# Performance work log

Measured on AMD Instinct MI355X. Metric: run time of the kernel, lower is better.

## Reference

```python
import jax, jax.numpy as jnp
import numpy as np

B, T, E = 2, 2048, 768
H = 12
HD = E // H          # 64
ROT = 32             # rotary dim (= head_dim // 2 in CLVP)
SCALE = HD ** -0.5


def rotate_half(x):
    # split last dim into (2, d/2), rotate second half by 90 deg
    x = x.reshape(*x.shape[:-1], 2, x.shape[-1] // 2)
    x1, x2 = x[..., 0, :], x[..., 1, :]
    return jnp.concatenate([-x2, x1], axis=-1)


def apply_rotary_pos_emb(state, freqs):
    # state: (B*H, T, HD); freqs: (1, T, ROT)
    pos_emb_len = freqs.shape[-1]
    s_l, s_r = state[..., :pos_emb_len], state[..., pos_emb_len:]
    f = freqs[:, :, -s_l.shape[-1]:]
    s_l = s_l * jnp.cos(f) + rotate_half(s_l) * jnp.sin(f)
    return jnp.concatenate([s_l, s_r], axis=-1)


def setup_inputs() -> dict:
    key = jax.random.key(0)
    ks = jax.random.split(key, 6)
    hidden_states = jax.random.normal(ks[0], (B, T, E), dtype=jnp.float32)
    rotary_pos_emb = jax.random.uniform(ks[1], (1, T, ROT), dtype=jnp.float32)
    Wq = jax.random.normal(ks[2], (E, E), dtype=jnp.float32) * 0.02
    Wk = jax.random.normal(ks[3], (E, E), dtype=jnp.float32) * 0.02
    Wv = jax.random.normal(ks[4], (E, E), dtype=jnp.float32) * 0.02
    Wo = jax.random.normal(ks[5], (E, E), dtype=jnp.float32) * 0.02
    bo = jnp.zeros((E,), dtype=jnp.float32)
    return {"hidden_states": hidden_states, "rotary_pos_emb": rotary_pos_emb,
            "Wq": Wq, "Wk": Wk, "Wv": Wv, "Wo": Wo, "bo": bo}


def _shape(x):
    # (B, T, E) -> (B*H, T, HD)
    return x.reshape(B, T, H, HD).transpose(0, 2, 1, 3).reshape(B * H, T, HD)


def reference(hidden_states, rotary_pos_emb, Wq, Wk, Wv, Wo, bo):
    # nn.Linear: x @ W.T
    q = _shape(hidden_states @ Wq.T * SCALE)
    k = _shape(hidden_states @ Wk.T)
    v = _shape(hidden_states @ Wv.T)

    q = apply_rotary_pos_emb(q, rotary_pos_emb)
    k = apply_rotary_pos_emb(k, rotary_pos_emb)
    v = apply_rotary_pos_emb(v, rotary_pos_emb)  # CLVP applies RoPE to V too

    attn = jax.nn.softmax(jnp.einsum('bqd,bkd->bqk', q, k), axis=-1)  # (B*H, T, T)
    out = jnp.einsum('bqk,bkd->bqd', attn, v)                          # (B*H, T, HD)
    out = out.reshape(B, H, T, HD).transpose(0, 2, 1, 3).reshape(B, T, E)
    return out @ Wo.T + bo
```

## Files before the change

kernel.cpp:

```cpp
#include <hip/hip_runtime.h>
#include <hip/hip_bf16.h>

typedef unsigned short ushort_t;
typedef __attribute__((ext_vector_type(8))) short short8;
typedef __attribute__((ext_vector_type(4))) float f32x4;

constexpr int B  = 2;
constexpr int T  = 2048;
constexpr int E  = 768;
constexpr int H  = 12;
constexpr int HD = 64;

__device__ __forceinline__ ushort_t f2bf(float x) {
  unsigned int u = __float_as_uint(x);
  u += 0x7fffu + ((u >> 16) & 1u);
  return (ushort_t)(u >> 16);
}

__device__ __forceinline__ unsigned int pack_bf2(float a, float b) {
  __hip_bfloat162 h = __float22bfloat162_rn(float2{a, b});
  return *(unsigned int*)&h;
}

__device__ __forceinline__ int swz(int row, int col) {
  return row * 64 + ((((col >> 3) ^ (row & 7)) << 3) | (col & 7));
}
__device__ __forceinline__ int swz32(int row, int col) {
  return row * 32 + ((((col >> 3) ^ (row & 3)) << 3) | (col & 7));
}

__global__ __launch_bounds__(256) void cvt_all(
    const float* __restrict__ X,  const float* __restrict__ Wq,
    const float* __restrict__ Wk, const float* __restrict__ Wv,
    const float* __restrict__ Wo, const float* __restrict__ rope,
    ushort_t* __restrict__ Xb,  ushort_t* __restrict__ Wqb,
    ushort_t* __restrict__ Wkb, ushort_t* __restrict__ Wvb,
    ushort_t* __restrict__ Wob, float* __restrict__ ct, float* __restrict__ st)
{
  constexpr int NX4 = (B * T * E) / 4;
  constexpr int NW4 = (E * E) / 4;
  constexpr int NC4 = NX4 + 4 * NW4;
  int i = blockIdx.x * 256 + threadIdx.x;
  if (i < NC4) {
    const float* s; ushort_t* d; int j;
    if (i < NX4) { s = X; d = Xb; j = i; }
    else {
      int t = i - NX4;
      int w = t / NW4; j = t - w * NW4;
      s = (w == 0) ? Wq : (w == 1) ? Wk : (w == 2) ? Wv : Wo;
      d = (w == 0) ? Wqb : (w == 1) ? Wkb : (w == 2) ? Wvb : Wob;
    }
    float4 v = ((const float4*)s)[j];
    ushort4 o;
    o.x = f2bf(v.x); o.y = f2bf(v.y); o.z = f2bf(v.z); o.w = f2bf(v.w);
    ((ushort4*)d)[j] = o;
  } else {
    int j = (i - NC4) * 4;
    float4 f = *(const float4*)(rope + j);
    float c, s;
    sincosf(f.x, &s, &c); ct[j+0] = c; st[j+0] = s;
    sincosf(f.y, &s, &c); ct[j+1] = c; st[j+1] = s;
    sincosf(f.z, &s, &c); ct[j+2] = c; st[j+2] = s;
    sincosf(f.w, &s, &c); ct[j+3] = c; st[j+3] = s;
  }
}

__global__ __launch_bounds__(256) void qkv_gemm(
    const ushort_t* __restrict__ Xb,
    const ushort_t* __restrict__ Wqb, const ushort_t* __restrict__ Wkb,
    const ushort_t* __restrict__ Wvb,
    const float* __restrict__ ct, const float* __restrict__ st,
    ushort_t* __restrict__ qb, ushort_t* __restrict__ kb, ushort_t* __restrict__ vtb)
{
  __shared__ __align__(16) ushort_t smem[64 * 132];
  ushort_t* Xs = smem;
  ushort_t* Ws = smem + 128 * 32;
  const int tid  = threadIdx.x;
  const int wave = tid >> 6;
  const int lane = tid & 63;
  const int l15  = lane & 15, quad = lane >> 4;
  const int n0 = blockIdx.x * 64;
  const int m0 = blockIdx.y * 128;
  const int z  = blockIdx.z;
  const ushort_t* Wt = (z == 0) ? Wqb : (z == 1) ? Wkb : Wvb;
  const int h = n0 >> 6;

  f32x4 acc[2][4];
  #pragma unroll
  for (int i = 0; i < 2; ++i)
    #pragma unroll
    for (int j = 0; j < 4; ++j) acc[i][j] = (f32x4){0.f, 0.f, 0.f, 0.f};

  const int srX = tid >> 1, scX = (tid & 1) * 16;
  const int srW = tid >> 2, scW = (tid & 3) * 8;

  for (int k0 = 0; k0 < E; k0 += 32) {
    uint4 xa = *(const uint4*)(Xb + (size_t)(m0 + srX) * E + k0 + scX);
    uint4 xc = *(const uint4*)(Xb + (size_t)(m0 + srX) * E + k0 + scX + 8);
    uint4 wa = *(const uint4*)(Wt + (size_t)(n0 + srW) * E + k0 + scW);
    *(uint4*)&Xs[swz32(srX, scX)]     = xa;
    *(uint4*)&Xs[swz32(srX, scX + 8)] = xc;
    *(uint4*)&Ws[swz32(srW, scW)]     = wa;
    __syncthreads();
    short8 a[2];
    #pragma unroll
    for (int mt = 0; mt < 2; ++mt)
      a[mt] = *(const short8*)&Xs[swz32(wave * 32 + mt * 16 + l15, quad * 8)];
    #pragma unroll
    for (int nt = 0; nt < 4; ++nt) {
      short8 bb = *(const short8*)&Ws[swz32(nt * 16 + l15, quad * 8)];
      #pragma unroll
      for (int mt = 0; mt < 2; ++mt)
        acc[mt][nt] = __builtin_amdgcn_mfma_f32_16x16x32_bf16(a[mt], bb, acc[mt][nt], 0, 0, 0);
    }
    __syncthreads();
  }

  const float qscale = (z == 0) ? 0.125f : 1.0f;
  if (z < 2) {
    #pragma unroll
    for (int mt = 0; mt < 2; ++mt) {
      #pragma unroll
      for (int r = 0; r < 4; ++r) {
        int mloc = wave * 32 + mt * 16 + quad * 4 + r;
        int t = (m0 + mloc) & (T - 1);
        float s0 = acc[mt][0][r] * qscale;
        float s1 = acc[mt][1][r] * qscale;
        float c0v = ct[t * 32 + l15],      sn0 = st[t * 32 + l15];
        float c1v = ct[t * 32 + 16 + l15], sn1 = st[t * 32 + 16 + l15];
        smem[mloc * 64 + l15]      = f2bf(s0 * c0v - s1 * sn0);
        smem[mloc * 64 + 16 + l15] = f2bf(s1 * c1v + s0 * sn1);
        smem[mloc * 64 + 32 + l15] = f2bf(acc[mt][2][r] * qscale);
        smem[mloc * 64 + 48 + l15] = f2bf(acc[mt][3][r] * qscale);
      }
    }
    __syncthreads();
    ushort_t* dst = (z == 0) ? qb : kb;
    int row = tid >> 1, half = (tid & 1) * 32;
    int m = m0 + row, b = m >> 11, t = m & (T - 1);
    size_t base = ((size_t)(b * H + h) * T + t) * HD + half;
    #pragma unroll
    for (int c = 0; c < 32; c += 8)
      *(uint4*)(dst + base + c) = *(const uint4*)&smem[row * 64 + half + c];
  } else {
    #pragma unroll
    for (int mt = 0; mt < 2; ++mt) {
      #pragma unroll
      for (int r = 0; r < 4; ++r) {
        int mloc = wave * 32 + mt * 16 + quad * 4 + r;
        int t = (m0 + mloc) & (T - 1);
        float s0 = acc[mt][0][r], s1 = acc[mt][1][r];
        float c0v = ct[t * 32 + l15],      sn0 = st[t * 32 + l15];
        float c1v = ct[t * 32 + 16 + l15], sn1 = st[t * 32 + 16 + l15];
        smem[(l15)      * 132 + mloc] = f2bf(s0 * c0v - s1 * sn0);
        smem[(16 + l15) * 132 + mloc] = f2bf(s1 * c1v + s0 * sn1);
        smem[(32 + l15) * 132 + mloc] = f2bf(acc[mt][2][r]);
        smem[(48 + l15) * 132 + mloc] = f2bf(acc[mt][3][r]);
      }
    }
    __syncthreads();
    int b = m0 >> 11, t0 = m0 & (T - 1);
    int d = tid >> 2, c0 = (tid & 3) * 32;
    size_t obase = ((size_t)(b * H + h) * HD + d) * (size_t)T + t0 + c0;
    #pragma unroll
    for (int c = 0; c < 32; c += 8)
      *(uint4*)(vtb + obase + c) = *(const uint4*)&smem[d * 132 + c0 + c];
  }
}

__global__ __launch_bounds__(256, 4) void attn_kernel(
    const ushort_t* __restrict__ qbuf, const ushort_t* __restrict__ kbuf,
    const ushort_t* __restrict__ vtbuf, ushort_t* __restrict__ cbuf)
{
  __shared__ __align__(16) ushort_t Ks[2][64 * 64];
  __shared__ __align__(16) ushort_t Vt[2][64 * 64];
  __shared__ __align__(16) ushort_t Ps[64 * 64];
  const int tid  = threadIdx.x;
  const int wave = tid >> 6;
  const int lane = tid & 63;
  const int l15  = lane & 15, quad = lane >> 4;
  const int q0 = blockIdx.x * 64;
  const int bh = blockIdx.y;
  const ushort_t* Qg = qbuf  + (size_t)bh * T * HD;
  const ushort_t* Kg = kbuf  + (size_t)bh * T * HD;
  const ushort_t* Vg = vtbuf + (size_t)bh * HD * T;

  short8 qa[2];
  #pragma unroll
  for (int hf = 0; hf < 2; ++hf)
    qa[hf] = *(const short8*)(Qg + (size_t)(q0 + wave * 16 + l15) * HD + hf * 32 + quad * 8);

  const int srow = tid >> 2, cb0 = (tid & 3) * 16;
  {
    uint4 ka = *(const uint4*)(Kg + (size_t)srow * HD + cb0);
    uint4 kc = *(const uint4*)(Kg + (size_t)srow * HD + cb0 + 8);
    uint4 va = *(const uint4*)(Vg + (size_t)srow * T + cb0);
    uint4 vc = *(const uint4*)(Vg + (size_t)srow * T + cb0 + 8);
    *(uint4*)&Ks[0][swz(srow, cb0)]     = ka;
    *(uint4*)&Ks[0][swz(srow, cb0 + 8)] = kc;
    *(uint4*)&Vt[0][swz(srow, cb0)]     = va;
    *(uint4*)&Vt[0][swz(srow, cb0 + 8)] = vc;
  }
  __syncthreads();

  f32x4 o[4];
  #pragma unroll
  for (int nt = 0; nt < 4; ++nt) o[nt] = (f32x4){0.f, 0.f, 0.f, 0.f};
  float lsum = 0.f;

  for (int kt = 0; kt < T; kt += 64) {
    const int cur = (kt >> 6) & 1;
    const bool more = (kt + 64) < T;
    uint4 nk0, nk1, nv0, nv1;
    if (more) {
      nk0 = *(const uint4*)(Kg + (size_t)(kt + 64 + srow) * HD + cb0);
      nk1 = *(const uint4*)(Kg + (size_t)(kt + 64 + srow) * HD + cb0 + 8);
      nv0 = *(const uint4*)(Vg + (size_t)srow * T + kt + 64 + cb0);
      nv1 = *(const uint4*)(Vg + (size_t)srow * T + kt + 64 + cb0 + 8);
    }

    f32x4 ss[4];
    #pragma unroll
    for (int mt = 0; mt < 4; ++mt) ss[mt] = (f32x4){0.f, 0.f, 0.f, 0.f};
    #pragma unroll
    for (int mt = 0; mt < 4; ++mt) {
      int row = mt * 16 + l15;
      short8 ka0 = *(const short8*)&Ks[cur][swz(row, quad * 8)];
      short8 ka1 = *(const short8*)&Ks[cur][swz(row, 32 + quad * 8)];
      ss[mt] = __builtin_amdgcn_mfma_f32_16x16x32_bf16(ka0, qa[0], ss[mt], 0, 0, 0);
      ss[mt] = __builtin_amdgcn_mfma_f32_16x16x32_bf16(ka1, qa[1], ss[mt], 0, 0, 0);
    }

    const int rp = wave * 16 + l15;
    #pragma unroll
    for (int mt = 0; mt < 4; ++mt) {
      float p0 = __expf(ss[mt][0]);
      float p1 = __expf(ss[mt][1]);
      float p2 = __expf(ss[mt][2]);
      float p3 = __expf(ss[mt][3]);
      lsum += (p0 + p1) + (p2 + p3);
      uint2 w2;
      w2.x = pack_bf2(p0, p1);
      w2.y = pack_bf2(p2, p3);
      *(uint2*)&Ps[swz(rp, mt * 16 + quad * 4)] = w2;
    }

    short8 pa0 = *(const short8*)&Ps[swz(rp, quad * 8)];
    short8 pa1 = *(const short8*)&Ps[swz(rp, 32 + quad * 8)];
    #pragma unroll
    for (int nt = 0; nt < 4; ++nt) {
      int vr = nt * 16 + l15;
      short8 vb0 = *(const short8*)&Vt[cur][swz(vr, quad * 8)];
      short8 vb1 = *(const short8*)&Vt[cur][swz(vr, 32 + quad * 8)];
      o[nt] = __builtin_amdgcn_mfma_f32_16x16x32_bf16(pa0, vb0, o[nt], 0, 0, 0);
      o[nt] = __builtin_amdgcn_mfma_f32_16x16x32_bf16(pa1, vb1, o[nt], 0, 0, 0);
    }

    if (more) {
      const int nxt = cur ^ 1;
      *(uint4*)&Ks[nxt][swz(srow, cb0)]     = nk0;
      *(uint4*)&Ks[nxt][swz(srow, cb0 + 8)] = nk1;
      *(uint4*)&Vt[nxt][swz(srow, cb0)]     = nv0;
      *(uint4*)&Vt[nxt][swz(srow, cb0 + 8)] = nv1;
    }
    __syncthreads();
  }

  lsum += __shfl_xor(lsum, 16);
  lsum += __shfl_xor(lsum, 32);

  const int b = bh / H, h = bh % H;
  #pragma unroll
  for (int r = 0; r < 4; ++r) {
    float lr = __shfl(lsum, quad * 4 + r);
    float inv = 1.0f / lr;
    int t = q0 + wave * 16 + quad * 4 + r;
    size_t base = ((size_t)b * T + t) * E + h * HD;
    cbuf[base + l15]      = f2bf(o[0][r] * inv);
    cbuf[base + 16 + l15] = f2bf(o[1][r] * inv);
    cbuf[base + 32 + l15] = f2bf(o[2][r] * inv);
    cbuf[base + 48 + l15] = f2bf(o[3][r] * inv);
  }
}

__global__ __launch_bounds__(256) void out_gemm(
    const ushort_t* __restrict__ Xc, const ushort_t* __restrict__ Wob,
    const float* __restrict__ bo, float* __restrict__ out)
{
  __shared__ __align__(16) ushort_t Xs[128][40];
  __shared__ __align__(16) ushort_t Ws[64][40];
  const int tid  = threadIdx.x;
  const int wave = tid >> 6;
  const int lane = tid & 63;
  const int l15  = lane & 15, quad = lane >> 4;
  const int n0 = blockIdx.x * 64;
  const int m0 = blockIdx.y * 128;

  f32x4 acc[2][4];
  #pragma unroll
  for (int i = 0; i < 2; ++i)
    #pragma unroll
    for (int j = 0; j < 4; ++j) acc[i][j] = (f32x4){0.f, 0.f, 0.f, 0.f};

  const int srX = tid >> 1, scX = (tid & 1) * 16;
  const int srW = tid >> 2, scW = (tid & 3) * 8;

  for (int k0 = 0; k0 < E; k0 += 32) {
    *(uint4*)&Xs[srX][scX]     = *(const uint4*)(Xc + (size_t)(m0 + srX) * E + k0 + scX);
    *(uint4*)&Xs[srX][scX + 8] = *(const uint4*)(Xc + (size_t)(m0 + srX) * E + k0 + scX + 8);
    *(uint4*)&Ws[srW][scW]     = *(const uint4*)(Wob + (size_t)(n0 + srW) * E + k0 + scW);
    __syncthreads();
    #pragma unroll
    for (int mt = 0; mt < 2; ++mt) {
      short8 a = *(const short8*)&Xs[wave * 32 + mt * 16 + l15][quad * 8];
      #pragma unroll
      for (int nt = 0; nt < 4; ++nt) {
        short8 bb = *(const short8*)&Ws[nt * 16 + l15][quad * 8];
        acc[mt][nt] = __builtin_amdgcn_mfma_f32_16x16x32_bf16(a, bb, acc[mt][nt], 0, 0, 0);
      }
    }
    __syncthreads();
  }

  float bias[4];
  #pragma unroll
  for (int nt = 0; nt < 4; ++nt) bias[nt] = bo[n0 + nt * 16 + l15];
  #pragma unroll
  for (int mt = 0; mt < 2; ++mt) {
    #pragma unroll
    for (int r = 0; r < 4; ++r) {
      int m = m0 + wave * 32 + mt * 16 + quad * 4 + r;
      float* op = out + (size_t)m * E + n0;
      op[l15]      = acc[mt][0][r] + bias[0];
      op[16 + l15] = acc[mt][1][r] + bias[1];
      op[32 + l15] = acc[mt][2][r] + bias[2];
      op[48 + l15] = acc[mt][3][r] + bias[3];
    }
  }
}

extern "C" void kernel_launch(void* const* d_in, const int* in_sizes, int n_in,
                              void* d_out, int out_size, void* d_ws, size_t ws_size,
                              hipStream_t stream) {
  (void)in_sizes; (void)n_in; (void)out_size; (void)ws_size;
  const float* X    = (const float*)d_in[0];
  const float* rope = (const float*)d_in[1];
  const float* Wq   = (const float*)d_in[2];
  const float* Wk   = (const float*)d_in[3];
  const float* Wv   = (const float*)d_in[4];
  const float* Wo   = (const float*)d_in[5];
  const float* bo   = (const float*)d_in[6];
  float* out = (float*)d_out;

  const size_t NX = (size_t)B * T * E;
  const size_t NW = (size_t)E * E;
  const size_t NR = (size_t)T * 32;
  ushort_t* Xb  = (ushort_t*)d_ws;
  ushort_t* Wqb = Xb  + NX;
  ushort_t* Wkb = Wqb + NW;
  ushort_t* Wvb = Wkb + NW;
  ushort_t* Wob = Wvb + NW;
  ushort_t* qb  = Wob + NW;
  ushort_t* kb  = qb  + NX;
  ushort_t* vtb = kb  + NX;
  ushort_t* cb  = vtb + NX;
  float* ct = (float*)(cb + NX);
  float* st = ct + NR;

  const int total4 = (int)((NX + 4 * NW + NR) / 4);
  cvt_all<<<total4 / 256, 256, 0, stream>>>(X, Wq, Wk, Wv, Wo, rope,
                                            Xb, Wqb, Wkb, Wvb, Wob, ct, st);

  qkv_gemm<<<dim3(E / 64, (B * T) / 128, 3), 256, 0, stream>>>(
      Xb, Wqb, Wkb, Wvb, ct, st, qb, kb, vtb);
  attn_kernel<<<dim3(T / 64, B * H), 256, 0, stream>>>(qb, kb, vtb, cb);
  out_gemm<<<dim3(E / 64, (B * T) / 128), 256, 0, stream>>>(cb, Wob, bo, out);
}
```

Baseline: 183.2 us.

## Store Q/K/V in MFMA fragment order and load attention operands directly to registers

The QKV GEMM epilogue now writes Q, K and V in a pre-swizzled per-lane MFMA fragment layout. This lets the attention kernel load its operands with coalesced 16-byte global loads straight into registers, instead of staging K and V through double-buffered shared memory. Block-wide barriers and most LDS traffic in the attention loop go away, leaving only a per-wave P buffer. In exchange, each wave re-reads K/V from global memory or L2 on its own, with no sharing within the block, and register pressure goes up from prefetching the next K tile.

```diff
diff --git a/kernel.cpp b/kernel.cpp
--- a/kernel.cpp
+++ b/kernel.cpp
@@ -70,7 +70,7 @@
     const ushort_t* __restrict__ Wqb, const ushort_t* __restrict__ Wkb,
     const ushort_t* __restrict__ Wvb,
     const float* __restrict__ ct, const float* __restrict__ st,
-    ushort_t* __restrict__ qb, ushort_t* __restrict__ kb, ushort_t* __restrict__ vtb)
+    ushort_t* __restrict__ qfb, ushort_t* __restrict__ kfb, ushort_t* __restrict__ vfb)
 {
   __shared__ __align__(16) ushort_t smem[64 * 132];
   ushort_t* Xs = smem;
@@ -116,7 +116,11 @@
     __syncthreads();
   }
 
+  const int b  = m0 >> 11;
+  const int t0 = m0 & (T - 1);
+  const int bh = b * H + h;
   const float qscale = (z == 0) ? 0.125f : 1.0f;
+
   if (z < 2) {
     #pragma unroll
     for (int mt = 0; mt < 2; ++mt) {
@@ -128,20 +132,36 @@
         float s1 = acc[mt][1][r] * qscale;
         float c0v = ct[t * 32 + l15],      sn0 = st[t * 32 + l15];
         float c1v = ct[t * 32 + 16 + l15], sn1 = st[t * 32 + 16 + l15];
-        smem[mloc * 64 + l15]      = f2bf(s0 * c0v - s1 * sn0);
-        smem[mloc * 64 + 16 + l15] = f2bf(s1 * c1v + s0 * sn1);
-        smem[mloc * 64 + 32 + l15] = f2bf(acc[mt][2][r] * qscale);
-        smem[mloc * 64 + 48 + l15] = f2bf(acc[mt][3][r] * qscale);
-      }
-    }
-    __syncthreads();
-    ushort_t* dst = (z == 0) ? qb : kb;
-    int row = tid >> 1, half = (tid & 1) * 32;
-    int m = m0 + row, b = m >> 11, t = m & (T - 1);
-    size_t base = ((size_t)(b * H + h) * T + t) * HD + half;
-    #pragma unroll
-    for (int c = 0; c < 32; c += 8)
-      *(uint4*)(dst + base + c) = *(const uint4*)&smem[row * 64 + half + c];
+        smem[swz(mloc, l15)]      = f2bf(s0 * c0v - s1 * sn0);
+        smem[swz(mloc, 16 + l15)] = f2bf(s1 * c1v + s0 * sn1);
+        smem[swz(mloc, 32 + l15)] = f2bf(acc[mt][2][r] * qscale);
+        smem[swz(mloc, 48 + l15)] = f2bf(acc[mt][3][r] * qscale);
+      }
+    }
+    __syncthreads();
+    if (z == 0) {
+      #pragma unroll
+      for (int i = 0; i < 4; ++i) {
+        int p = tid + 256 * i;
+        int qtl = p >> 7, kh = (p >> 6) & 1, ln = p & 63;
+        int tl = qtl * 16 + (ln & 15);
+        int d  = kh * 32 + (ln >> 4) * 8;
+        uint4 v = *(const uint4*)&smem[swz(tl, d)];
+        size_t off = ((size_t)((bh * 128 + (t0 >> 4) + qtl) * 2 + kh)) * 512 + ln * 8;
+        *(uint4*)(qfb + off) = v;
+      }
+    } else {
+      #pragma unroll
+      for (int i = 0; i < 4; ++i) {
+        int p = tid + 256 * i;
+        int ktl = p >> 9, mt = (p >> 7) & 3, kh = (p >> 6) & 1, ln = p & 63;
+        int tl = ktl * 64 + mt * 16 + (ln & 15);
+        int d  = kh * 32 + (ln >> 4) * 8;
+        uint4 v = *(const uint4*)&smem[swz(tl, d)];
+        size_t off = ((size_t)(((bh * 32 + (t0 >> 6) + ktl) * 4 + mt) * 2 + kh)) * 512 + ln * 8;
+        *(uint4*)(kfb + off) = v;
+      }
+    }
   } else {
     #pragma unroll
     for (int mt = 0; mt < 2; ++mt) {
@@ -159,79 +179,75 @@
       }
     }
     __syncthreads();
-    int b = m0 >> 11, t0 = m0 & (T - 1);
-    int d = tid >> 2, c0 = (tid & 3) * 32;
-    size_t obase = ((size_t)(b * H + h) * HD + d) * (size_t)T + t0 + c0;
-    #pragma unroll
-    for (int c = 0; c < 32; c += 8)
-      *(uint4*)(vtb + obase + c) = *(const uint4*)&smem[d * 132 + c0 + c];
-  }
-}
-
-__global__ __launch_bounds__(256, 4) void attn_kernel(
-    const ushort_t* __restrict__ qbuf, const ushort_t* __restrict__ kbuf,
-    const ushort_t* __restrict__ vtbuf, ushort_t* __restrict__ cbuf)
+    #pragma unroll
+    for (int i = 0; i < 4; ++i) {
+      int p = tid + 256 * i;
+      int ktl = p >> 9, nt = (p >> 7) & 3, kh = (p >> 6) & 1, ln = p & 63;
+      int d  = nt * 16 + (ln & 15);
+      int tl = ktl * 64 + kh * 32 + (ln >> 4) * 8;
+      uint4 v = *(const uint4*)&smem[d * 132 + tl];
+      size_t off = ((size_t)(((bh * 32 + (t0 >> 6) + ktl) * 4 + nt) * 2 + kh)) * 512 + ln * 8;
+      *(uint4*)(vfb + off) = v;
+    }
+  }
+}
+
+__global__ __launch_bounds__(256) void attn_kernel(
+    const ushort_t* __restrict__ qfb, const ushort_t* __restrict__ kfb,
+    const ushort_t* __restrict__ vfb, ushort_t* __restrict__ cbuf)
 {
-  __shared__ __align__(16) ushort_t Ks[2][64 * 64];
-  __shared__ __align__(16) ushort_t Vt[2][64 * 64];
-  __shared__ __align__(16) ushort_t Ps[64 * 64];
+  __shared__ __align__(16) ushort_t Ps[4][16 * 64];
   const int tid  = threadIdx.x;
   const int wave = tid >> 6;
   const int lane = tid & 63;
   const int l15  = lane & 15, quad = lane >> 4;
   const int q0 = blockIdx.x * 64;
   const int bh = blockIdx.y;
-  const ushort_t* Qg = qbuf  + (size_t)bh * T * HD;
-  const ushort_t* Kg = kbuf  + (size_t)bh * T * HD;
-  const ushort_t* Vg = vtbuf + (size_t)bh * HD * T;
+  const ushort_t* Qf = qfb + (size_t)bh * (T * HD);
+  const ushort_t* Kf = kfb + (size_t)bh * (T * HD);
+  const ushort_t* Vf = vfb + (size_t)bh * (T * HD);
+  ushort_t* Pw = &Ps[wave][0];
 
   short8 qa[2];
   #pragma unroll
-  for (int hf = 0; hf < 2; ++hf)
-    qa[hf] = *(const short8*)(Qg + (size_t)(q0 + wave * 16 + l15) * HD + hf * 32 + quad * 8);
-
-  const int srow = tid >> 2, cb0 = (tid & 3) * 16;
-  {
-    uint4 ka = *(const uint4*)(Kg + (size_t)srow * HD + cb0);
-    uint4 kc = *(const uint4*)(Kg + (size_t)srow * HD + cb0 + 8);
-    uint4 va = *(const uint4*)(Vg + (size_t)srow * T + cb0);
-    uint4 vc = *(const uint4*)(Vg + (size_t)srow * T + cb0 + 8);
-    *(uint4*)&Ks[0][swz(srow, cb0)]     = ka;
-    *(uint4*)&Ks[0][swz(srow, cb0 + 8)] = kc;
-    *(uint4*)&Vt[0][swz(srow, cb0)]     = va;
-    *(uint4*)&Vt[0][swz(srow, cb0 + 8)] = vc;
-  }
-  __syncthreads();
+  for (int kh = 0; kh < 2; ++kh)
+    qa[kh] = *(const short8*)(Qf + ((size_t)(((q0 >> 4) + wave) * 2 + kh)) * 512 + lane * 8);
+
+  short8 ka[4][2];
+  #pragma unroll
+  for (int mt = 0; mt < 4; ++mt)
+    #pragma unroll
+    for (int kh = 0; kh < 2; ++kh)
+      ka[mt][kh] = *(const short8*)(Kf + ((size_t)(mt * 2 + kh)) * 512 + lane * 8);
 
   f32x4 o[4];
   #pragma unroll
   for (int nt = 0; nt < 4; ++nt) o[nt] = (f32x4){0.f, 0.f, 0.f, 0.f};
   float lsum = 0.f;
 
-  for (int kt = 0; kt < T; kt += 64) {
-    const int cur = (kt >> 6) & 1;
-    const bool more = (kt + 64) < T;
-    uint4 nk0, nk1, nv0, nv1;
-    if (more) {
-      nk0 = *(const uint4*)(Kg + (size_t)(kt + 64 + srow) * HD + cb0);
-      nk1 = *(const uint4*)(Kg + (size_t)(kt + 64 + srow) * HD + cb0 + 8);
-      nv0 = *(const uint4*)(Vg + (size_t)srow * T + kt + 64 + cb0);
-      nv1 = *(const uint4*)(Vg + (size_t)srow * T + kt + 64 + cb0 + 8);
-    }
+  for (int kt = 0; kt < T / 64; ++kt) {
+    short8 va[4][2], kn[4][2];
+    #pragma unroll
+    for (int nt = 0; nt < 4; ++nt)
+      #pragma unroll
+      for (int kh = 0; kh < 2; ++kh)
+        va[nt][kh] = *(const short8*)(Vf + ((size_t)((kt * 4 + nt) * 2 + kh)) * 512 + lane * 8);
+    const int ktn = (kt + 1 < T / 64) ? kt + 1 : kt;
+    #pragma unroll
+    for (int mt = 0; mt < 4; ++mt)
+      #pragma unroll
+      for (int kh = 0; kh < 2; ++kh)
+        kn[mt][kh] = *(const short8*)(Kf + ((size_t)((ktn * 4 + mt) * 2 + kh)) * 512 + lane * 8);
 
     f32x4 ss[4];
     #pragma unroll
     for (int mt = 0; mt < 4; ++mt) ss[mt] = (f32x4){0.f, 0.f, 0.f, 0.f};
     #pragma unroll
     for (int mt = 0; mt < 4; ++mt) {
-      int row = mt * 16 + l15;
-      short8 ka0 = *(const short8*)&Ks[cur][swz(row, quad * 8)];
-      short8 ka1 = *(const short8*)&Ks[cur][swz(row, 32 + quad * 8)];
-      ss[mt] = __builtin_amdgcn_mfma_f32_16x16x32_bf16(ka0, qa[0], ss[mt], 0, 0, 0);
-      ss[mt] = __builtin_amdgcn_mfma_f32_16x16x32_bf16(ka1, qa[1], ss[mt], 0, 0, 0);
-    }
-
-    const int rp = wave * 16 + l15;
+      ss[mt] = __builtin_amdgcn_mfma_f32_16x16x32_bf16(ka[mt][0], qa[0], ss[mt], 0, 0, 0);
+      ss[mt] = __builtin_amdgcn_mfma_f32_16x16x32_bf16(ka[mt][1], qa[1], ss[mt], 0, 0, 0);
+    }
+
     #pragma unroll
     for (int mt = 0; mt < 4; ++mt) {
       float p0 = __expf(ss[mt][0]);
@@ -242,28 +258,22 @@
       uint2 w2;
       w2.x = pack_bf2(p0, p1);
       w2.y = pack_bf2(p2, p3);
-      *(uint2*)&Ps[swz(rp, mt * 16 + quad * 4)] = w2;
-    }
-
-    short8 pa0 = *(const short8*)&Ps[swz(rp, quad * 8)];
-    short8 pa1 = *(const short8*)&Ps[swz(rp, 32 + quad * 8)];
+      *(uint2*)&Pw[swz(l15, mt * 16 + quad * 4)] = w2;
+    }
+
+    short8 pa0 = *(const short8*)&Pw[swz(l15, quad * 8)];
+    short8 pa1 = *(const short8*)&Pw[swz(l15, 32 + quad * 8)];
     #pragma unroll
     for (int nt = 0; nt < 4; ++nt) {
-      int vr = nt * 16 + l15;
-      short8 vb0 = *(const short8*)&Vt[cur][swz(vr, quad * 8)];
-      short8 vb1 = *(const short8*)&Vt[cur][swz(vr, 32 + quad * 8)];
-      o[nt] = __builtin_amdgcn_mfma_f32_16x16x32_bf16(pa0, vb0, o[nt], 0, 0, 0);
-      o[nt] = __builtin_amdgcn_mfma_f32_16x16x32_bf16(pa1, vb1, o[nt], 0, 0, 0);
-    }
-
-    if (more) {
-      const int nxt = cur ^ 1;
-      *(uint4*)&Ks[nxt][swz(srow, cb0)]     = nk0;
-      *(uint4*)&Ks[nxt][swz(srow, cb0 + 8)] = nk1;
-      *(uint4*)&Vt[nxt][swz(srow, cb0)]     = nv0;
-      *(uint4*)&Vt[nxt][swz(srow, cb0 + 8)] = nv1;
-    }
-    __syncthreads();
+      o[nt] = __builtin_amdgcn_mfma_f32_16x16x32_bf16(pa0, va[nt][0], o[nt], 0, 0, 0);
+      o[nt] = __builtin_amdgcn_mfma_f32_16x16x32_bf16(pa1, va[nt][1], o[nt], 0, 0, 0);
+    }
+
+    #pragma unroll
+    for (int mt = 0; mt < 4; ++mt) {
+      ka[mt][0] = kn[mt][0];
+      ka[mt][1] = kn[mt][1];
+    }
   }
 
   lsum += __shfl_xor(lsum, 16);
@@ -360,10 +370,10 @@
   ushort_t* Wkb = Wqb + NW;
   ushort_t* Wvb = Wkb + NW;
   ushort_t* Wob = Wvb + NW;
-  ushort_t* qb  = Wob + NW;
-  ushort_t* kb  = qb  + NX;
-  ushort_t* vtb = kb  + NX;
-  ushort_t* cb  = vtb + NX;
+  ushort_t* qfb = Wob + NW;
+  ushort_t* kfb = qfb + NX;
+  ushort_t* vfb = kfb + NX;
+  ushort_t* cb  = vfb + NX;
   float* ct = (float*)(cb + NX);
   float* st = ct + NR;
 
@@ -372,7 +382,7 @@
                                             Xb, Wqb, Wkb, Wvb, Wob, ct, st);
 
   qkv_gemm<<<dim3(E / 64, (B * T) / 128, 3), 256, 0, stream>>>(
-      Xb, Wqb, Wkb, Wvb, ct, st, qb, kb, vtb);
-  attn_kernel<<<dim3(T / 64, B * H), 256, 0, stream>>>(qb, kb, vtb, cb);
+      Xb, Wqb, Wkb, Wvb, ct, st, qfb, kfb, vfb);
+  attn_kernel<<<dim3(T / 64, B * H), 256, 0, stream>>>(qfb, kfb, vfb, cb);
   out_gemm<<<dim3(E / 64, (B * T) / 128), 256, 0, stream>>>(cb, Wob, bo, out);
 }
```

Result: no change. 185.3 us (+1.2%).

## Enlarge QKV GEMM tile to 128x128 with K=64 steps and swizzle out_gemm LDS

Applied to the files above, without the earlier changes.

The QKV projection GEMM now computes a 128x128 output tile per block (two heads) with a 2x2 wave layout and a K step of 64. Each wave accumulates a 64x64 sub-tile, which raises MFMA work per LDS load and halves the number of K-loop barriers. The epilogues are reworked so one block writes both heads, including the transposed V layout through two LDS regions. out_gemm also moves to a K step of 64 with XOR-swizzled LDS in place of padded arrays. The cost is more registers and LDS per block and half as many QKV blocks, which may reduce occupancy and the number of CUs kept busy.

```diff
diff --git a/kernel.cpp b/kernel.cpp
--- a/kernel.cpp
+++ b/kernel.cpp
@@ -24,9 +24,6 @@
 
 __device__ __forceinline__ int swz(int row, int col) {
   return row * 64 + ((((col >> 3) ^ (row & 7)) << 3) | (col & 7));
-}
-__device__ __forceinline__ int swz32(int row, int col) {
-  return row * 32 + ((((col >> 3) ^ (row & 3)) << 3) | (col & 7));
 }
 
 __global__ __launch_bounds__(256) void cvt_all(
@@ -72,99 +69,119 @@
     const float* __restrict__ ct, const float* __restrict__ st,
     ushort_t* __restrict__ qb, ushort_t* __restrict__ kb, ushort_t* __restrict__ vtb)
 {
-  __shared__ __align__(16) ushort_t smem[64 * 132];
+  __shared__ __align__(16) ushort_t smem[128 * 132];
   ushort_t* Xs = smem;
-  ushort_t* Ws = smem + 128 * 32;
+  ushort_t* Ws = smem + 128 * 64;
   const int tid  = threadIdx.x;
   const int wave = tid >> 6;
   const int lane = tid & 63;
   const int l15  = lane & 15, quad = lane >> 4;
-  const int n0 = blockIdx.x * 64;
+  const int ww = wave >> 1, wn = wave & 1;
+  const int n0 = blockIdx.x * 128;
   const int m0 = blockIdx.y * 128;
   const int z  = blockIdx.z;
   const ushort_t* Wt = (z == 0) ? Wqb : (z == 1) ? Wkb : Wvb;
-  const int h = n0 >> 6;
-
-  f32x4 acc[2][4];
-  #pragma unroll
-  for (int i = 0; i < 2; ++i)
+  const int h0 = n0 >> 6;
+
+  f32x4 acc[4][4];
+  #pragma unroll
+  for (int i = 0; i < 4; ++i)
     #pragma unroll
     for (int j = 0; j < 4; ++j) acc[i][j] = (f32x4){0.f, 0.f, 0.f, 0.f};
 
-  const int srX = tid >> 1, scX = (tid & 1) * 16;
-  const int srW = tid >> 2, scW = (tid & 3) * 8;
-
-  for (int k0 = 0; k0 < E; k0 += 32) {
-    uint4 xa = *(const uint4*)(Xb + (size_t)(m0 + srX) * E + k0 + scX);
-    uint4 xc = *(const uint4*)(Xb + (size_t)(m0 + srX) * E + k0 + scX + 8);
-    uint4 wa = *(const uint4*)(Wt + (size_t)(n0 + srW) * E + k0 + scW);
-    *(uint4*)&Xs[swz32(srX, scX)]     = xa;
-    *(uint4*)&Xs[swz32(srX, scX + 8)] = xc;
-    *(uint4*)&Ws[swz32(srW, scW)]     = wa;
-    __syncthreads();
-    short8 a[2];
-    #pragma unroll
-    for (int mt = 0; mt < 2; ++mt)
-      a[mt] = *(const short8*)&Xs[swz32(wave * 32 + mt * 16 + l15, quad * 8)];
+  const int srow = tid >> 1, sc = (tid & 1) * 32;
+
+  for (int k0 = 0; k0 < E; k0 += 64) {
+    uint4 x0 = *(const uint4*)(Xb + (size_t)(m0 + srow) * E + k0 + sc);
+    uint4 x1 = *(const uint4*)(Xb + (size_t)(m0 + srow) * E + k0 + sc + 8);
+    uint4 x2 = *(const uint4*)(Xb + (size_t)(m0 + srow) * E + k0 + sc + 16);
+    uint4 x3 = *(const uint4*)(Xb + (size_t)(m0 + srow) * E + k0 + sc + 24);
+    uint4 w0 = *(const uint4*)(Wt + (size_t)(n0 + srow) * E + k0 + sc);
+    uint4 w1 = *(const uint4*)(Wt + (size_t)(n0 + srow) * E + k0 + sc + 8);
+    uint4 w2 = *(const uint4*)(Wt + (size_t)(n0 + srow) * E + k0 + sc + 16);
+    uint4 w3 = *(const uint4*)(Wt + (size_t)(n0 + srow) * E + k0 + sc + 24);
+    *(uint4*)&Xs[swz(srow, sc)]      = x0;
+    *(uint4*)&Xs[swz(srow, sc + 8)]  = x1;
+    *(uint4*)&Xs[swz(srow, sc + 16)] = x2;
+    *(uint4*)&Xs[swz(srow, sc + 24)] = x3;
+    *(uint4*)&Ws[swz(srow, sc)]      = w0;
+    *(uint4*)&Ws[swz(srow, sc + 8)]  = w1;
+    *(uint4*)&Ws[swz(srow, sc + 16)] = w2;
+    *(uint4*)&Ws[swz(srow, sc + 24)] = w3;
+    __syncthreads();
+    short8 a[4][2];
+    #pragma unroll
+    for (int mt = 0; mt < 4; ++mt)
+      #pragma unroll
+      for (int kh = 0; kh < 2; ++kh)
+        a[mt][kh] = *(const short8*)&Xs[swz(ww * 64 + mt * 16 + l15, kh * 32 + quad * 8)];
     #pragma unroll
     for (int nt = 0; nt < 4; ++nt) {
-      short8 bb = *(const short8*)&Ws[swz32(nt * 16 + l15, quad * 8)];
-      #pragma unroll
-      for (int mt = 0; mt < 2; ++mt)
-        acc[mt][nt] = __builtin_amdgcn_mfma_f32_16x16x32_bf16(a[mt], bb, acc[mt][nt], 0, 0, 0);
-    }
-    __syncthreads();
-  }
-
+      #pragma unroll
+      for (int kh = 0; kh < 2; ++kh) {
+        short8 bb = *(const short8*)&Ws[swz(wn * 64 + nt * 16 + l15, kh * 32 + quad * 8)];
+        #pragma unroll
+        for (int mt = 0; mt < 4; ++mt)
+          acc[mt][nt] = __builtin_amdgcn_mfma_f32_16x16x32_bf16(a[mt][kh], bb, acc[mt][nt], 0, 0, 0);
+      }
+    }
+    __syncthreads();
+  }
+
+  const int b  = m0 >> 11;
+  const int t0 = m0 & (T - 1);
   const float qscale = (z == 0) ? 0.125f : 1.0f;
+
   if (z < 2) {
     #pragma unroll
-    for (int mt = 0; mt < 2; ++mt) {
+    for (int mt = 0; mt < 4; ++mt) {
       #pragma unroll
       for (int r = 0; r < 4; ++r) {
-        int mloc = wave * 32 + mt * 16 + quad * 4 + r;
-        int t = (m0 + mloc) & (T - 1);
+        int tl = ww * 64 + mt * 16 + quad * 4 + r;
+        int t  = t0 + tl;
         float s0 = acc[mt][0][r] * qscale;
         float s1 = acc[mt][1][r] * qscale;
         float c0v = ct[t * 32 + l15],      sn0 = st[t * 32 + l15];
         float c1v = ct[t * 32 + 16 + l15], sn1 = st[t * 32 + 16 + l15];
-        smem[mloc * 64 + l15]      = f2bf(s0 * c0v - s1 * sn0);
-        smem[mloc * 64 + 16 + l15] = f2bf(s1 * c1v + s0 * sn1);
-        smem[mloc * 64 + 32 + l15] = f2bf(acc[mt][2][r] * qscale);
-        smem[mloc * 64 + 48 + l15] = f2bf(acc[mt][3][r] * qscale);
+        ushort_t* row = smem + tl * 132 + wn * 64;
+        row[l15]      = f2bf(s0 * c0v - s1 * sn0);
+        row[16 + l15] = f2bf(s1 * c1v + s0 * sn1);
+        row[32 + l15] = f2bf(acc[mt][2][r] * qscale);
+        row[48 + l15] = f2bf(acc[mt][3][r] * qscale);
       }
     }
     __syncthreads();
     ushort_t* dst = (z == 0) ? qb : kb;
-    int row = tid >> 1, half = (tid & 1) * 32;
-    int m = m0 + row, b = m >> 11, t = m & (T - 1);
-    size_t base = ((size_t)(b * H + h) * T + t) * HD + half;
-    #pragma unroll
-    for (int c = 0; c < 32; c += 8)
-      *(uint4*)(dst + base + c) = *(const uint4*)&smem[row * 64 + half + c];
+    int row = tid >> 1, half = tid & 1;
+    int t = t0 + row, h = h0 + half;
+    size_t base = ((size_t)(b * H + h) * T + t) * HD;
+    #pragma unroll
+    for (int c = 0; c < 64; c += 8)
+      *(uint4*)(dst + base + c) = *(const uint4*)&smem[row * 132 + half * 64 + c];
   } else {
-    #pragma unroll
-    for (int mt = 0; mt < 2; ++mt) {
+    ushort_t* Tv = smem + wn * (64 * 132);
+    #pragma unroll
+    for (int mt = 0; mt < 4; ++mt) {
       #pragma unroll
       for (int r = 0; r < 4; ++r) {
-        int mloc = wave * 32 + mt * 16 + quad * 4 + r;
-        int t = (m0 + mloc) & (T - 1);
+        int tl = ww * 64 + mt * 16 + quad * 4 + r;
+        int t  = t0 + tl;
         float s0 = acc[mt][0][r], s1 = acc[mt][1][r];
         float c0v = ct[t * 32 + l15],      sn0 = st[t * 32 + l15];
         float c1v = ct[t * 32 + 16 + l15], sn1 = st[t * 32 + 16 + l15];
-        smem[(l15)      * 132 + mloc] = f2bf(s0 * c0v - s1 * sn0);
-        smem[(16 + l15) * 132 + mloc] = f2bf(s1 * c1v + s0 * sn1);
-        smem[(32 + l15) * 132 + mloc] = f2bf(acc[mt][2][r]);
-        smem[(48 + l15) * 132 + mloc] = f2bf(acc[mt][3][r]);
+        Tv[(l15)      * 132 + tl] = f2bf(s0 * c0v - s1 * sn0);
+        Tv[(16 + l15) * 132 + tl] = f2bf(s1 * c1v + s0 * sn1);
+        Tv[(32 + l15) * 132 + tl] = f2bf(acc[mt][2][r]);
+        Tv[(48 + l15) * 132 + tl] = f2bf(acc[mt][3][r]);
       }
     }
     __syncthreads();
-    int b = m0 >> 11, t0 = m0 & (T - 1);
-    int d = tid >> 2, c0 = (tid & 3) * 32;
-    size_t obase = ((size_t)(b * H + h) * HD + d) * (size_t)T + t0 + c0;
-    #pragma unroll
-    for (int c = 0; c < 32; c += 8)
-      *(uint4*)(vtb + obase + c) = *(const uint4*)&smem[d * 132 + c0 + c];
+    int hh = tid >> 7, d = (tid >> 1) & 63, c0 = (tid & 1) * 64;
+    const ushort_t* Trh = smem + hh * (64 * 132);
+    size_t obase = ((size_t)(b * H + h0 + hh) * HD + d) * (size_t)T + t0 + c0;
+    #pragma unroll
+    for (int c = 0; c < 64; c += 8)
+      *(uint4*)(vtb + obase + c) = *(const uint4*)&Trh[d * 132 + c0 + c];
   }
 }
 
@@ -287,8 +304,8 @@
     const ushort_t* __restrict__ Xc, const ushort_t* __restrict__ Wob,
     const float* __restrict__ bo, float* __restrict__ out)
 {
-  __shared__ __align__(16) ushort_t Xs[128][40];
-  __shared__ __align__(16) ushort_t Ws[64][40];
+  __shared__ __align__(16) ushort_t Xs[128 * 64];
+  __shared__ __align__(16) ushort_t Ws[64 * 64];
   const int tid  = threadIdx.x;
   const int wave = tid >> 6;
   const int lane = tid & 63;
@@ -302,21 +319,37 @@
     #pragma unroll
     for (int j = 0; j < 4; ++j) acc[i][j] = (f32x4){0.f, 0.f, 0.f, 0.f};
 
-  const int srX = tid >> 1, scX = (tid & 1) * 16;
-  const int srW = tid >> 2, scW = (tid & 3) * 8;
-
-  for (int k0 = 0; k0 < E; k0 += 32) {
-    *(uint4*)&Xs[srX][scX]     = *(const uint4*)(Xc + (size_t)(m0 + srX) * E + k0 + scX);
-    *(uint4*)&Xs[srX][scX + 8] = *(const uint4*)(Xc + (size_t)(m0 + srX) * E + k0 + scX + 8);
-    *(uint4*)&Ws[srW][scW]     = *(const uint4*)(Wob + (size_t)(n0 + srW) * E + k0 + scW);
-    __syncthreads();
-    #pragma unroll
-    for (int mt = 0; mt < 2; ++mt) {
-      short8 a = *(const short8*)&Xs[wave * 32 + mt * 16 + l15][quad * 8];
-      #pragma unroll
-      for (int nt = 0; nt < 4; ++nt) {
-        short8 bb = *(const short8*)&Ws[nt * 16 + l15][quad * 8];
-        acc[mt][nt] = __builtin_amdgcn_mfma_f32_16x16x32_bf16(a, bb, acc[mt][nt], 0, 0, 0);
+  const int srX = tid >> 1, scX = (tid & 1) * 32;
+  const int srW = tid >> 2, scW = (tid & 3) * 16;
+
+  for (int k0 = 0; k0 < E; k0 += 64) {
+    uint4 x0 = *(const uint4*)(Xc + (size_t)(m0 + srX) * E + k0 + scX);
+    uint4 x1 = *(const uint4*)(Xc + (size_t)(m0 + srX) * E + k0 + scX + 8);
+    uint4 x2 = *(const uint4*)(Xc + (size_t)(m0 + srX) * E + k0 + scX + 16);
+    uint4 x3 = *(const uint4*)(Xc + (size_t)(m0 + srX) * E + k0 + scX + 24);
+    uint4 w0 = *(const uint4*)(Wob + (size_t)(n0 + srW) * E + k0 + scW);
+    uint4 w1 = *(const uint4*)(Wob + (size_t)(n0 + srW) * E + k0 + scW + 8);
+    *(uint4*)&Xs[swz(srX, scX)]      = x0;
+    *(uint4*)&Xs[swz(srX, scX + 8)]  = x1;
+    *(uint4*)&Xs[swz(srX, scX + 16)] = x2;
+    *(uint4*)&Xs[swz(srX, scX + 24)] = x3;
+    *(uint4*)&Ws[swz(srW, scW)]      = w0;
+    *(uint4*)&Ws[swz(srW, scW + 8)]  = w1;
+    __syncthreads();
+    short8 a[2][2];
+    #pragma unroll
+    for (int mt = 0; mt < 2; ++mt)
+      #pragma unroll
+      for (int kh = 0; kh < 2; ++kh)
+        a[mt][kh] = *(const short8*)&Xs[swz(wave * 32 + mt * 16 + l15, kh * 32 + quad * 8)];
+    #pragma unroll
+    for (int nt = 0; nt < 4; ++nt) {
+      #pragma unroll
+      for (int kh = 0; kh < 2; ++kh) {
+        short8 bb = *(const short8*)&Ws[swz(nt * 16 + l15, kh * 32 + quad * 8)];
+        #pragma unroll
+        for (int mt = 0; mt < 2; ++mt)
+          acc[mt][nt] = __builtin_amdgcn_mfma_f32_16x16x32_bf16(a[mt][kh], bb, acc[mt][nt], 0, 0, 0);
       }
     }
     __syncthreads();
@@ -371,7 +404,7 @@
   cvt_all<<<total4 / 256, 256, 0, stream>>>(X, Wq, Wk, Wv, Wo, rope,
                                             Xb, Wqb, Wkb, Wvb, Wob, ct, st);
 
-  qkv_gemm<<<dim3(E / 64, (B * T) / 128, 3), 256, 0, stream>>>(
+  qkv_gemm<<<dim3(E / 128, (B * T) / 128, 3), 256, 0, stream>>>(
       Xb, Wqb, Wkb, Wvb, ct, st, qb, kb, vtb);
   attn_kernel<<<dim3(T / 64, B * H), 256, 0, stream>>>(qb, kb, vtb, cb);
   out_gemm<<<dim3(E / 64, (B * T) / 128), 256, 0, stream>>>(cb, Wob, bo, out);
```

Result: no change. 182.3 us (-0.5%).
